# Kernel tuning notes

Hardware: AMD Instinct MI355X
Metric: run time of the kernel (lower is better)

## Reference

```python
import jax, jax.numpy as jnp
import numpy as np

N_NODES = 50000
N_EDGES = 800000
DIM = 64


def _param(key, shape, scale):
    return jax.random.normal(key, shape, dtype=jnp.float32) * scale


def setup_inputs() -> dict:
    key = jax.random.key(0)
    ks = jax.random.split(key, 20)
    s = 1.0 / np.sqrt(DIM)
    x = jax.random.normal(ks[0], (N_NODES, DIM), dtype=jnp.float32)
    weights = jax.random.uniform(ks[1], (6,), dtype=jnp.float32)
    edge_index = jax.random.randint(ks[2], (2, N_EDGES), 0, N_NODES, dtype=jnp.int64)
    return {
        "x": x,
        "weights": weights,
        # mlp
        "W_mlp": _param(ks[3], (DIM, DIM), s), "b_mlp": jnp.zeros((DIM,), jnp.float32),
        # sage (mean aggregator): lin_l on neighbor mean, lin_r on self
        "Wl_sage": _param(ks[4], (DIM, DIM), s), "Wr_sage": _param(ks[5], (DIM, DIM), s),
        "b_sage": jnp.zeros((DIM,), jnp.float32),
        # gcn
        "W_gcn": _param(ks[6], (DIM, DIM), s), "b_gcn": jnp.zeros((DIM,), jnp.float32),
        # gat (single head)
        "W_gat": _param(ks[7], (DIM, DIM), s),
        "a_src": _param(ks[8], (DIM,), s), "a_dst": _param(ks[9], (DIM,), s),
        "b_gat": jnp.zeros((DIM,), jnp.float32),
        # chebconv K=3
        "W_cheb": _param(ks[10], (3, DIM, DIM), s), "b_cheb": jnp.zeros((DIM,), jnp.float32),
        # gin (eps=0, nn = Linear)
        "W_gin": _param(ks[11], (DIM, DIM), s), "b_gin": jnp.zeros((DIM,), jnp.float32),
        "edge_index": edge_index,
    }


def _mixed_forward(x, weights, W_mlp, b_mlp, Wl_sage, Wr_sage, b_sage,
                   W_gcn, b_gcn, W_gat, a_src, a_dst, b_gat,
                   W_cheb, b_cheb, W_gin, b_gin, edge_index):
    N = x.shape[0]
    src, dst = edge_index[0], edge_index[1]
    seg_sum = lambda v, idx: jax.ops.segment_sum(v, idx, num_segments=N)

    deg = seg_sum(jnp.ones(src.shape[0], x.dtype), dst)  # in-degree [N]
    nsum = seg_sum(x[src], dst)                           # sum of neighbor feats [N, D]

    # --- mlp (graph-free) ---
    o_mlp = x @ W_mlp + b_mlp

    # --- sage, mean aggregation ---
    nmean = nsum / jnp.maximum(deg, 1.0)[:, None]
    o_sage = nmean @ Wl_sage + x @ Wr_sage + b_sage

    # --- gcn with self loops: D'^{-1/2} (A+I) D'^{-1/2} X W ---
    dinv = jax.lax.rsqrt(deg + 1.0)
    xw = x @ W_gcn
    norm_e = dinv[src] * dinv[dst]
    o_gcn = seg_sum(norm_e[:, None] * xw[src], dst) + xw * (dinv * dinv)[:, None] + b_gcn

    # --- gat, single head, self loops appended, leaky_relu(0.2) scoring ---
    h = x @ W_gat
    el, er = h @ a_src, h @ a_dst
    loop = jnp.arange(N, dtype=src.dtype)
    src2 = jnp.concatenate([src, loop])
    dst2 = jnp.concatenate([dst, loop])
    e = jax.nn.leaky_relu(el[src2] + er[dst2], 0.2)
    m = jax.ops.segment_max(e, dst2, num_segments=N)
    p = jnp.exp(e - m[dst2])
    z = jax.ops.segment_sum(p, dst2, num_segments=N)
    alpha = p / (z[dst2] + 1e-16)
    o_gat = jax.ops.segment_sum(alpha[:, None] * h[src2], dst2, num_segments=N) + b_gat

    # --- cheb K=3, lambda_max=2: L_hat = L_norm - I = -A_norm ---
    dinv_c = jax.lax.rsqrt(jnp.maximum(deg, 1.0))
    nrm = dinv_c[src] * dinv_c[dst]
    prop = lambda t: seg_sum(nrm[:, None] * t[src], dst)
    T0 = x
    T1 = -prop(T0)
    T2 = -2.0 * prop(T1) - T0
    o_cheb = T0 @ W_cheb[0] + T1 @ W_cheb[1] + T2 @ W_cheb[2] + b_cheb

    # --- gin, eps=0, nn = Linear ---
    o_gin = (x + nsum) @ W_gin + b_gin

    outs = (o_mlp, o_sage, o_gcn, o_gat, o_cheb, o_gin)
    res = jnp.zeros_like(o_mlp)
    for k, o in enumerate(outs):
        res = res + weights[k] * jax.nn.elu(o)
    return res


def reference(x, weights, W_mlp, b_mlp, Wl_sage, Wr_sage, b_sage,
              W_gcn, b_gcn, W_gat, a_src, a_dst, b_gat,
              W_cheb, b_cheb, W_gin, b_gin, edge_index):
    return _mixed_forward(x, weights, W_mlp, b_mlp, Wl_sage, Wr_sage, b_sage,
                          W_gcn, b_gcn, W_gat, a_src, a_dst, b_gat,
                          W_cheb, b_cheb, W_gin, b_gin, edge_index)
```

## Files before the change

### kernel.cpp

```cpp
#include <hip/hip_runtime.h>
#include <cstdint>
#include <cstddef>

#define NN 50000
#define NE 800000
#define CAP 96
#define NSEG 8
#define SEGW 6250

constexpr size_t O_CNT   = 0;
constexpr size_t O_SLOT  = 50048;
constexpr size_t O_NODAL = O_SLOT + (size_t)NN*CAP;
constexpr size_t O_VA    = O_NODAL + 200000;
constexpr size_t O_VB    = O_VA + 64;
constexpr size_t O_XB    = O_VB + 64;
constexpr size_t O_NSB   = O_XB + 1600032;
constexpr size_t O_T1B   = O_NSB + 1600000;
constexpr size_t O_V1B   = O_T1B + 1600032;
constexpr size_t O_GB    = O_V1B + 1600000;
constexpr size_t O_UB    = O_GB  + 1600000;
constexpr size_t O_WPK   = O_UB  + 1600000;

typedef __attribute__((ext_vector_type(8))) short short8;
typedef __attribute__((ext_vector_type(4))) float f32x4;

__device__ __forceinline__ float leaky02(float v){ return v >= 0.f ? v : 0.2f*v; }
__device__ __forceinline__ float eluf(float v){ return v > 0.f ? v : (__expf(v) - 1.f); }

__device__ __forceinline__ void lds_fence(){
  asm volatile("s_waitcnt lgkmcnt(0)" ::: "memory");
}

__device__ __forceinline__ unsigned short f2bf(float f){
  unsigned u = __float_as_uint(f);
  unsigned r = (u + 0x7FFFu + ((u >> 16) & 1u)) >> 16;
  return (unsigned short)r;
}
__device__ __forceinline__ float bf2f(unsigned short b){
  return __uint_as_float(((unsigned)b) << 16);
}
__device__ __forceinline__ unsigned pack2(unsigned short lo, unsigned short hi){
  return (unsigned)lo | ((unsigned)hi << 16);
}

__global__ __launch_bounds__(256) void k_scatter(
    const int* __restrict__ src, const int* __restrict__ dst,
    int* __restrict__ cnt, unsigned short* __restrict__ slot,
    const float* __restrict__ W_mlp, const float* __restrict__ Wr,
    const float* __restrict__ W_cheb, const float* __restrict__ W_gin,
    const float* __restrict__ Wl, const float* __restrict__ W_gcn,
    const float* __restrict__ W_gat,
    const float* __restrict__ a_src, const float* __restrict__ a_dst,
    const float4* __restrict__ x4,
    float* __restrict__ va, float* __restrict__ vb,
    unsigned short* __restrict__ wpk,
    ushort4* __restrict__ xb4, ushort4* __restrict__ t1b4){
  int b = blockIdx.x;
  int seg = b & (NSEG-1);
  int lo = seg * SEGW;
  int e = (b >> 3)*256 + threadIdx.x;
  if (e < NE){
    int d = dst[e];
    if (d >= lo && d < lo + SEGW){
      int s = src[e];
      int pos = atomicAdd(&cnt[d], 1);
      if (pos < CAP) slot[(size_t)d*CAP + pos] = (unsigned short)s;
    }
  }
  if (b == 0){
    int k = threadIdx.x;
    if (k < 64){
      float sa = 0.f, sb = 0.f;
      for (int j = 0; j < 64; ++j){
        float w = W_gat[k*64 + j];
        sa = fmaf(w, a_src[j], sa);
        sb = fmaf(w, a_dst[j], sb);
      }
      va[k] = sa; vb[k] = sb;
    }
  } else if (b <= 9){
    int w = b - 1;
    const float* s; const float* sub = nullptr;
    switch (w){
      case 0: s = W_mlp; break;
      case 1: s = Wr; break;
      case 2: s = W_cheb; sub = W_cheb + 8192; break;
      case 3: s = W_gin; break;
      case 4: s = Wl; break;
      case 5: s = W_cheb + 4096; break;
      case 6: s = W_cheb + 8192; break;
      case 7: s = W_gcn; break;
      default: s = W_gat; break;
    }
    for (int ee = threadIdx.x; ee < 4096; ee += 256){
      int k = ee >> 6, n = ee & 63;
      float f = s[ee];
      if (sub) f -= sub[ee];
      wpk[(size_t)w*4096 + (size_t)n*64 + k] = f2bf(f);
    }
  } else if (b < 3136){
    int i = (b - 10)*256 + threadIdx.x;
    if (i < NN*16){
      float4 v = x4[i];
      ushort4 o;
      o.x = f2bf(v.x); o.y = f2bf(v.y); o.z = f2bf(v.z); o.w = f2bf(v.w);
      xb4[i] = o;
    } else if (i < (NN+1)*16){
      ushort4 z; z.x = 0; z.y = 0; z.z = 0; z.w = 0;
      xb4[i] = z;
      t1b4[i] = z;
    }
  }
}

__global__ __launch_bounds__(256) void k_nodal(const float* __restrict__ x,
    const int* __restrict__ cnt, const float* __restrict__ va, const float* __restrict__ vb,
    float4* __restrict__ nodal){
  int tid = threadIdx.x;
  int li = tid & 15;
  int row = blockIdx.x*16 + (tid >> 4);
  if (row >= NN) return;
  float4 hv = *(const float4*)&x[(size_t)row*64 + li*4];
  float4 av = *(const float4*)&va[li*4];
  float4 bv = *(const float4*)&vb[li*4];
  float ps = hv.x*av.x + hv.y*av.y + hv.z*av.z + hv.w*av.w;
  float pd = hv.x*bv.x + hv.y*bv.y + hv.z*bv.z + hv.w*bv.w;
  #pragma unroll
  for (int o = 1; o < 16; o <<= 1){ ps += __shfl_xor(ps, o); pd += __shfl_xor(pd, o); }
  if (li == 0){
    float c = (float)cnt[row];
    float dinv  = rsqrtf(c + 1.f);
    float dinvc = rsqrtf(fmaxf(c, 1.f));
    nodal[row] = make_float4(dinvc, dinv, ps, pd);
  }
}

__global__ __launch_bounds__(256) void k_aggA(const float* __restrict__ x,
    const unsigned short* __restrict__ xb,
    const int* __restrict__ cnt, const unsigned short* __restrict__ slot,
    const float4* __restrict__ nodal,
    unsigned* __restrict__ nsb2, unsigned* __restrict__ t1b2,
    unsigned* __restrict__ v1b2, unsigned* __restrict__ gb2){
  __shared__ float4 sW[4][64];
  int wid  = threadIdx.x >> 6;
  int lane = threadIdx.x & 63;
  int node = blockIdx.x*4 + wid;
  if (node >= NN) return;
  int c = min(cnt[node], CAP);
  const unsigned short* sl = slot + (size_t)node*CAP;
  float4 nn = nodal[node];
  float ern = nn.w;
  int half = lane >> 5, hl = lane & 31;
  float a0e=0.f,a0o=0.f,a1e=0.f,a1o=0.f,a2e=0.f,a2o=0.f,a3e=0.f,a3o=0.f, zl=0.f;
  for (int base = 0; base < c; base += 64){
    int rem = min(64, c - base);
    bool act = lane < rem;
    int s = act ? (int)sl[base+lane] : NN;
    float4 ns = act ? nodal[s] : make_float4(0.f,0.f,0.f,0.f);
    float p = act ? __expf(fminf(leaky02(ns.z + ern), 60.f)) : 0.f;
    zl += p;
    sW[wid][lane] = make_float4(__int_as_float(s), ns.x, ns.y, p);
    lds_fence();
    for (int j = 0; j < rem; j += 8){
      float4 w[4]; unsigned uv[4];
      #pragma unroll
      for (int q2 = 0; q2 < 4; ++q2){
        w[q2] = sW[wid][j + 2*q2 + half];
        int sb = __float_as_int(w[q2].x);
        sb = ((unsigned)sb <= (unsigned)NN) ? sb : NN;
        uv[q2] = *(const unsigned*)&xb[(size_t)sb*64 + 2*hl];
      }
      #pragma unroll
      for (int q2 = 0; q2 < 4; ++q2){
        float lo = __uint_as_float(uv[q2] << 16);
        float hi = __uint_as_float(uv[q2] & 0xffff0000u);
        a0e += lo;                       a0o += hi;
        a1e = fmaf(w[q2].y, lo, a1e);    a1o = fmaf(w[q2].y, hi, a1o);
        a2e = fmaf(w[q2].z, lo, a2e);    a2o = fmaf(w[q2].z, hi, a2o);
        a3e = fmaf(w[q2].w, lo, a3e);    a3o = fmaf(w[q2].w, hi, a3o);
      }
    }
    lds_fence();
  }
  a0e += __shfl_xor(a0e, 32); a0o += __shfl_xor(a0o, 32);
  a1e += __shfl_xor(a1e, 32); a1o += __shfl_xor(a1o, 32);
  a2e += __shfl_xor(a2e, 32); a2o += __shfl_xor(a2o, 32);
  a3e += __shfl_xor(a3e, 32); a3o += __shfl_xor(a3o, 32);
  #pragma unroll
  for (int o = 32; o > 0; o >>= 1) zl += __shfl_xor(zl, o);
  float2 xs = *(const float2*)&x[(size_t)node*64 + 2*hl];
  float p_self = __expf(fminf(leaky02(nn.z + nn.w), 60.f));
  float rz = 1.f / (zl + p_self + 1e-16f);
  size_t off2 = (size_t)node*32 + hl;
  if (half == 0){
    nsb2[off2] = pack2(f2bf(a0e), f2bf(a0o));
    t1b2[off2] = pack2(f2bf(-nn.x*a1e), f2bf(-nn.x*a1o));
  } else {
    v1b2[off2] = pack2(f2bf(nn.y*a2e + nn.y*nn.y*xs.x), f2bf(nn.y*a2o + nn.y*nn.y*xs.y));
    gb2[off2]  = pack2(f2bf((a3e + p_self*xs.x)*rz), f2bf((a3o + p_self*xs.y)*rz));
  }
}

__global__ __launch_bounds__(256) void k_aggB(const unsigned short* __restrict__ t1b,
    const int* __restrict__ cnt, const unsigned short* __restrict__ slot,
    const float4* __restrict__ nodal, unsigned* __restrict__ ub2){
  __shared__ float2 sW[4][64];
  int wid  = threadIdx.x >> 6;
  int lane = threadIdx.x & 63;
  int node = blockIdx.x*4 + wid;
  if (node >= NN) return;
  int c = min(cnt[node], CAP);
  const unsigned short* sl = slot + (size_t)node*CAP;
  const float* nf = (const float*)nodal;
  int half = lane >> 5, hl = lane & 31;
  float ae = 0.f, ao = 0.f;
  for (int base = 0; base < c; base += 64){
    int rem = min(64, c - base);
    bool act = lane < rem;
    int s = act ? (int)sl[base+lane] : NN;
    float dc = act ? nf[(size_t)s*4] : 0.f;
    sW[wid][lane] = make_float2(__int_as_float(s), dc);
    lds_fence();
    for (int j = 0; j < rem; j += 8){
      float2 w[4]; unsigned uv[4];
      #pragma unroll
      for (int q2 = 0; q2 < 4; ++q2){
        w[q2] = sW[wid][j + 2*q2 + half];
        int sb = __float_as_int(w[q2].x);
        sb = ((unsigned)sb <= (unsigned)NN) ? sb : NN;
        uv[q2] = *(const unsigned*)&t1b[(size_t)sb*64 + 2*hl];
      }
      #pragma unroll
      for (int q2 = 0; q2 < 4; ++q2){
        float lo = __uint_as_float(uv[q2] << 16);
        float hi = __uint_as_float(uv[q2] & 0xffff0000u);
        ae = fmaf(w[q2].y, lo, ae);
        ao = fmaf(w[q2].y, hi, ao);
      }
    }
    lds_fence();
  }
  ae += __shfl_xor(ae, 32);
  ao += __shfl_xor(ao, 32);
  if (half == 0){
    float sc = -2.f * nodal[node].x;
    ub2[(size_t)node*32 + hl] = pack2(f2bf(sc*ae), f2bf(sc*ao));
  }
}

__global__ __launch_bounds__(64) void k_epi(
    const float* __restrict__ wts,
    const float* __restrict__ b_mlp, const float* __restrict__ b_sage,
    const float* __restrict__ b_gcn, const float* __restrict__ b_gat,
    const float* __restrict__ b_cheb, const float* __restrict__ b_gin,
    const float4* __restrict__ nodal, const unsigned short* __restrict__ wpk,
    const unsigned short* __restrict__ xb, const unsigned short* __restrict__ nsb,
    const unsigned short* __restrict__ t1b, const unsigned short* __restrict__ v1b,
    const unsigned short* __restrict__ gb, const unsigned short* __restrict__ ub,
    float* __restrict__ out){
  const int lane = threadIdx.x;
  const int ml   = lane & 15;
  const int q    = lane >> 4;
  const int rowbase = blockIdx.x*16;
  const float w0 = wts[0], w1 = wts[1], w2 = wts[2], w3 = wts[3], w4 = wts[4], w5 = wts[5];
  const float* nod = (const float*)nodal;

  short8 ah0, ah1;

  auto loadA = [&](const unsigned short* __restrict__ src){
    const unsigned short* p = src + (size_t)(rowbase + ml)*64 + q*8;
    ah0 = *(const short8*)p;
    ah1 = *(const short8*)(p + 32);
  };
  auto group = [&](int w, f32x4 acc[4]){
    const unsigned short* base = wpk + (size_t)w*4096;
    #pragma unroll
    for (int nt = 0; nt < 4; ++nt){
      const unsigned short* bp = base + (size_t)(nt*16 + ml)*64;
      short8 b0 = *(const short8*)(bp + q*8);
      short8 b1 = *(const short8*)(bp + 32 + q*8);
      acc[nt] = __builtin_amdgcn_mfma_f32_16x16x32_bf16(ah0, b0, acc[nt], 0, 0, 0);
      acc[nt] = __builtin_amdgcn_mfma_f32_16x16x32_bf16(ah1, b1, acc[nt], 0, 0, 0);
    }
  };

  f32x4 res[4];
  #pragma unroll
  for (int i = 0; i < 4; ++i) res[i] = (f32x4){0.f,0.f,0.f,0.f};

  auto emit = [&](const f32x4 acc[4], const float* __restrict__ bias, float wk){
    #pragma unroll
    for (int nt = 0; nt < 4; ++nt){
      float b = bias[nt*16 + ml];
      #pragma unroll
      for (int r = 0; r < 4; ++r) res[nt][r] += wk * eluf(acc[nt][r] + b);
    }
  };

  f32x4 t[4], accC[4], accWr[4], accG[4];

  loadA(v1b);
  #pragma unroll
  for (int i=0;i<4;++i) t[i] = (f32x4){0.f,0.f,0.f,0.f};
  group(7, t); emit(t, b_gcn, w2);
  loadA(gb);
  #pragma unroll
  for (int i=0;i<4;++i) t[i] = (f32x4){0.f,0.f,0.f,0.f};
  group(8, t); emit(t, b_gat, w3);
  loadA(ub);
  #pragma unroll
  for (int i=0;i<4;++i) accC[i] = (f32x4){0.f,0.f,0.f,0.f};
  group(6, accC);
  loadA(t1b);
  group(5, accC);
  loadA(xb);
  #pragma unroll
  for (int i=0;i<4;++i) t[i] = (f32x4){0.f,0.f,0.f,0.f};
  group(0, t); emit(t, b_mlp, w0);
  #pragma unroll
  for (int i=0;i<4;++i) accWr[i] = (f32x4){0.f,0.f,0.f,0.f};
  group(1, accWr);
  group(2, accC); emit(accC, b_cheb, w4);
  #pragma unroll
  for (int i=0;i<4;++i) accG[i] = (f32x4){0.f,0.f,0.f,0.f};
  group(3, accG);
  loadA(nsb);
  group(3, accG); emit(accG, b_gin, w5);
  #pragma unroll
  for (int i=0;i<4;++i) t[i] = (f32x4){0.f,0.f,0.f,0.f};
  group(4, t);
  #pragma unroll
  for (int nt = 0; nt < 4; ++nt){
    float b = b_sage[nt*16 + ml];
    #pragma unroll
    for (int r = 0; r < 4; ++r){
      int row = rowbase + q*4 + r;
      float dc = nod[(size_t)row*4];
      float invd = dc*dc;
      res[nt][r] += w1 * eluf(invd*t[nt][r] + accWr[nt][r] + b);
    }
  }
  #pragma unroll
  for (int nt = 0; nt < 4; ++nt){
    int col = nt*16 + ml;
    #pragma unroll
    for (int r = 0; r < 4; ++r){
      int row = rowbase + q*4 + r;
      out[(size_t)row*64 + col] = res[nt][r];
    }
  }
}

extern "C" void kernel_launch(void* const* d_in, const int* in_sizes, int n_in,
                              void* d_out, int out_size, void* d_ws, size_t ws_size,
                              hipStream_t stream){
  const float* x      = (const float*)d_in[0];
  const float* wts    = (const float*)d_in[1];
  const float* W_mlp  = (const float*)d_in[2];
  const float* b_mlp  = (const float*)d_in[3];
  const float* Wl     = (const float*)d_in[4];
  const float* Wr     = (const float*)d_in[5];
  const float* b_sage = (const float*)d_in[6];
  const float* W_gcn  = (const float*)d_in[7];
  const float* b_gcn  = (const float*)d_in[8];
  const float* W_gat  = (const float*)d_in[9];
  const float* a_src  = (const float*)d_in[10];
  const float* a_dst  = (const float*)d_in[11];
  const float* b_gat  = (const float*)d_in[12];
  const float* W_cheb = (const float*)d_in[13];
  const float* b_cheb = (const float*)d_in[14];
  const float* W_gin  = (const float*)d_in[15];
  const float* b_gin  = (const float*)d_in[16];
  const int*   ei     = (const int*)d_in[17];

  float* wsf  = (float*)d_ws;
  int*  cnt   = (int*)d_ws;
  unsigned short* slot = (unsigned short*)(wsf + O_SLOT);
  float4* nodal = (float4*)(wsf + O_NODAL);
  float* va   = wsf + O_VA;
  float* vb   = wsf + O_VB;
  unsigned short* xbu = (unsigned short*)(wsf + O_XB);
  unsigned short* nsb = (unsigned short*)(wsf + O_NSB);
  unsigned short* t1b = (unsigned short*)(wsf + O_T1B);
  unsigned short* v1b = (unsigned short*)(wsf + O_V1B);
  unsigned short* gb  = (unsigned short*)(wsf + O_GB);
  unsigned short* ub  = (unsigned short*)(wsf + O_UB);
  unsigned short* wpk = (unsigned short*)(wsf + O_WPK);
  float* out  = (float*)d_out;

  hipMemsetAsync(cnt, 0, NN*sizeof(int), stream);
  k_scatter <<<25000,256, 0, stream>>>(ei, ei + NE, cnt, slot,
                                       W_mlp, Wr, W_cheb, W_gin, Wl, W_gcn, W_gat,
                                       a_src, a_dst, (const float4*)x,
                                       va, vb, wpk, (ushort4*)xbu, (ushort4*)t1b);
  k_nodal   <<<3125, 256, 0, stream>>>(x, cnt, va, vb, nodal);
  k_aggA    <<<12500,256, 0, stream>>>(x, xbu, cnt, slot, nodal,
                                       (unsigned*)nsb, (unsigned*)t1b,
                                       (unsigned*)v1b, (unsigned*)gb);
  k_aggB    <<<12500,256, 0, stream>>>(t1b, cnt, slot, nodal, (unsigned*)ub);
  k_epi     <<<3125,  64, 0, stream>>>(wts, b_mlp, b_sage, b_gcn, b_gat, b_cheb, b_gin,
                                       nodal, wpk, xbu, nsb, t1b, v1b, gb, ub, out);
}
```

Baseline: 228.1 us.

## Map two nodes per wavefront in aggregation kernels, one per half-wave

The gather-aggregation kernels now assign one destination node to each 32-lane half of a wavefront instead of one node per full wavefront, halving the grid size. Each half-wave loads up to 32 neighbor indices and walks its own neighbor list. This removes the cross-half shuffle reduction and the idle half-wave stores. Average in-degree is about 16, so the old layout left most lanes idle in the neighbor-load phase. The loop now runs to the larger of the two nodes' degrees, so the half with fewer neighbors does padded iterations.

```diff
diff --git a/kernel.cpp b/kernel.cpp
--- a/kernel.cpp
+++ b/kernel.cpp
@@ -144,28 +144,29 @@
   __shared__ float4 sW[4][64];
   int wid  = threadIdx.x >> 6;
   int lane = threadIdx.x & 63;
-  int node = blockIdx.x*4 + wid;
-  if (node >= NN) return;
+  int half = lane >> 5, hl = lane & 31;
+  int node = blockIdx.x*8 + wid*2 + half;
   int c = min(cnt[node], CAP);
+  int cmax = max(c, __shfl_xor(c, 32));
   const unsigned short* sl = slot + (size_t)node*CAP;
   float4 nn = nodal[node];
   float ern = nn.w;
-  int half = lane >> 5, hl = lane & 31;
   float a0e=0.f,a0o=0.f,a1e=0.f,a1o=0.f,a2e=0.f,a2o=0.f,a3e=0.f,a3o=0.f, zl=0.f;
-  for (int base = 0; base < c; base += 64){
-    int rem = min(64, c - base);
-    bool act = lane < rem;
-    int s = act ? (int)sl[base+lane] : NN;
+  for (int base = 0; base < cmax; base += 32){
+    int rem = c - base;
+    bool act = hl < rem;
+    int s = act ? (int)sl[base+hl] : NN;
     float4 ns = act ? nodal[s] : make_float4(0.f,0.f,0.f,0.f);
     float p = act ? __expf(fminf(leaky02(ns.z + ern), 60.f)) : 0.f;
     zl += p;
     sW[wid][lane] = make_float4(__int_as_float(s), ns.x, ns.y, p);
     lds_fence();
-    for (int j = 0; j < rem; j += 8){
+    int remw = min(32, cmax - base);
+    for (int j = 0; j < remw; j += 4){
       float4 w[4]; unsigned uv[4];
       #pragma unroll
       for (int q2 = 0; q2 < 4; ++q2){
-        w[q2] = sW[wid][j + 2*q2 + half];
+        w[q2] = sW[wid][half*32 + j + q2];
         int sb = __float_as_int(w[q2].x);
         sb = ((unsigned)sb <= (unsigned)NN) ? sb : NN;
         uv[q2] = *(const unsigned*)&xb[(size_t)sb*64 + 2*hl];
@@ -182,23 +183,16 @@
     }
     lds_fence();
   }
-  a0e += __shfl_xor(a0e, 32); a0o += __shfl_xor(a0o, 32);
-  a1e += __shfl_xor(a1e, 32); a1o += __shfl_xor(a1o, 32);
-  a2e += __shfl_xor(a2e, 32); a2o += __shfl_xor(a2o, 32);
-  a3e += __shfl_xor(a3e, 32); a3o += __shfl_xor(a3o, 32);
-  #pragma unroll
-  for (int o = 32; o > 0; o >>= 1) zl += __shfl_xor(zl, o);
+  #pragma unroll
+  for (int o = 1; o <= 16; o <<= 1) zl += __shfl_xor(zl, o);
   float2 xs = *(const float2*)&x[(size_t)node*64 + 2*hl];
   float p_self = __expf(fminf(leaky02(nn.z + nn.w), 60.f));
   float rz = 1.f / (zl + p_self + 1e-16f);
   size_t off2 = (size_t)node*32 + hl;
-  if (half == 0){
-    nsb2[off2] = pack2(f2bf(a0e), f2bf(a0o));
-    t1b2[off2] = pack2(f2bf(-nn.x*a1e), f2bf(-nn.x*a1o));
-  } else {
-    v1b2[off2] = pack2(f2bf(nn.y*a2e + nn.y*nn.y*xs.x), f2bf(nn.y*a2o + nn.y*nn.y*xs.y));
-    gb2[off2]  = pack2(f2bf((a3e + p_self*xs.x)*rz), f2bf((a3o + p_self*xs.y)*rz));
-  }
+  nsb2[off2] = pack2(f2bf(a0e), f2bf(a0o));
+  t1b2[off2] = pack2(f2bf(-nn.x*a1e), f2bf(-nn.x*a1o));
+  v1b2[off2] = pack2(f2bf(nn.y*a2e + nn.y*nn.y*xs.x), f2bf(nn.y*a2o + nn.y*nn.y*xs.y));
+  gb2[off2]  = pack2(f2bf((a3e + p_self*xs.x)*rz), f2bf((a3o + p_self*xs.y)*rz));
 }
 
 __global__ __launch_bounds__(256) void k_aggB(const unsigned short* __restrict__ t1b,
@@ -207,25 +201,26 @@
   __shared__ float2 sW[4][64];
   int wid  = threadIdx.x >> 6;
   int lane = threadIdx.x & 63;
-  int node = blockIdx.x*4 + wid;
-  if (node >= NN) return;
+  int half = lane >> 5, hl = lane & 31;
+  int node = blockIdx.x*8 + wid*2 + half;
   int c = min(cnt[node], CAP);
+  int cmax = max(c, __shfl_xor(c, 32));
   const unsigned short* sl = slot + (size_t)node*CAP;
   const float* nf = (const float*)nodal;
-  int half = lane >> 5, hl = lane & 31;
   float ae = 0.f, ao = 0.f;
-  for (int base = 0; base < c; base += 64){
-    int rem = min(64, c - base);
-    bool act = lane < rem;
-    int s = act ? (int)sl[base+lane] : NN;
+  for (int base = 0; base < cmax; base += 32){
+    int rem = c - base;
+    bool act = hl < rem;
+    int s = act ? (int)sl[base+hl] : NN;
     float dc = act ? nf[(size_t)s*4] : 0.f;
     sW[wid][lane] = make_float2(__int_as_float(s), dc);
     lds_fence();
-    for (int j = 0; j < rem; j += 8){
+    int remw = min(32, cmax - base);
+    for (int j = 0; j < remw; j += 4){
       float2 w[4]; unsigned uv[4];
       #pragma unroll
       for (int q2 = 0; q2 < 4; ++q2){
-        w[q2] = sW[wid][j + 2*q2 + half];
+        w[q2] = sW[wid][half*32 + j + q2];
         int sb = __float_as_int(w[q2].x);
         sb = ((unsigned)sb <= (unsigned)NN) ? sb : NN;
         uv[q2] = *(const unsigned*)&t1b[(size_t)sb*64 + 2*hl];
@@ -240,12 +235,8 @@
     }
     lds_fence();
   }
-  ae += __shfl_xor(ae, 32);
-  ao += __shfl_xor(ao, 32);
-  if (half == 0){
-    float sc = -2.f * nodal[node].x;
-    ub2[(size_t)node*32 + hl] = pack2(f2bf(sc*ae), f2bf(sc*ao));
-  }
+  float sc = -2.f * nodal[node].x;
+  ub2[(size_t)node*32 + hl] = pack2(f2bf(sc*ae), f2bf(sc*ao));
 }
 
 __global__ __launch_bounds__(64) void k_epi(
@@ -394,10 +385,10 @@
                                        a_src, a_dst, (const float4*)x,
                                        va, vb, wpk, (ushort4*)xbu, (ushort4*)t1b);
   k_nodal   <<<3125, 256, 0, stream>>>(x, cnt, va, vb, nodal);
-  k_aggA    <<<12500,256, 0, stream>>>(x, xbu, cnt, slot, nodal,
+  k_aggA    <<<6250, 256, 0, stream>>>(x, xbu, cnt, slot, nodal,
                                        (unsigned*)nsb, (unsigned*)t1b,
                                        (unsigned*)v1b, (unsigned*)gb);
-  k_aggB    <<<12500,256, 0, stream>>>(t1b, cnt, slot, nodal, (unsigned*)ub);
+  k_aggB    <<<6250, 256, 0, stream>>>(t1b, cnt, slot, nodal, (unsigned*)ub);
   k_epi     <<<3125,  64, 0, stream>>>(wts, b_mlp, b_sage, b_gcn, b_gat, b_cheb, b_gin,
                                        nodal, wpk, xbu, nsb, t1b, v1b, gb, ub, out);
 }
```

New measurement: 219.5 us. -3.8%, faster.
